# Kernel optimization log

Hardware: AMD Instinct MI355X
Metric: run time of the kernel (lower is better)

## Reference

```python
import jax, jax.numpy as jnp
import numpy as np

GRID_SIZE = 5
SPLINE_ORDER = 3
COEFF = GRID_SIZE + SPLINE_ORDER  # 8 spline coefficients per (out,in) pair
NUM_HEADS = 4
NUM_LAYERS = 4
DIM = 256
FF_DIM = 1024
VOCAB = 32000
EPS_EMB = 1e-12   # layernorm_eps from init
EPS_LN = 1e-5     # nn.LayerNorm default inside encoder layers


def make_grid(in_features):
    # uniform extended B-spline grid over [-1, 1], shape (in, grid_size + 2*order + 1)
    h = 2.0 / GRID_SIZE
    g = jnp.arange(-SPLINE_ORDER, GRID_SIZE + SPLINE_ORDER + 1, dtype=jnp.float32) * h - 1.0
    return jnp.broadcast_to(g, (in_features, g.shape[0]))


def b_splines(x, grid):
    # Cox-de Boor recursion. x: (..., in) -> (..., in, COEFF)
    xe = x[..., None]
    bases = ((xe >= grid[:, :-1]) & (xe < grid[:, 1:])).astype(x.dtype)
    for k in range(1, SPLINE_ORDER + 1):
        left = (xe - grid[:, : -(k + 1)]) / (grid[:, k:-1] - grid[:, : -(k + 1)])
        right = (grid[:, k + 1:] - xe) / (grid[:, k + 1:] - grid[:, 1:-k])
        bases = left * bases[..., :-1] + right * bases[..., 1:]
    return bases


def kan(x, base_w, spline_w):
    # efficient-kan KANLinear: silu base path + B-spline path
    grid = make_grid(x.shape[-1])
    base = jax.nn.silu(x) @ base_w.T
    spl = b_splines(x, grid)                      # (..., in, COEFF)
    return base + jnp.einsum('...ic,oic->...o', spl, spline_w)


def layer_norm(x, g=None, b=None, eps=EPS_LN):
    mu = jnp.mean(x, axis=-1, keepdims=True)
    var = jnp.mean((x - mu) ** 2, axis=-1, keepdims=True)
    y = (x - mu) * jax.lax.rsqrt(var + eps)
    return y * g + b if g is not None else y


def setup_inputs() -> dict:
    key = jax.random.key(0)
    ks = iter(jax.random.split(key, 64))

    def w(shape, s=0.02):
        return jax.random.normal(next(ks), shape, jnp.float32) * s

    inp = {
        'input_ids': jax.random.randint(next(ks), (2, 512), 0, VOCAB),
        'word_emb': w((VOCAB, DIM)),
        'tok_type_emb': w((2, DIM)),
        'pos_emb': w((512, DIM)),
        'emb_ln_g': jnp.ones((DIM,), jnp.float32),
        'emb_ln_b': jnp.zeros((DIM,), jnp.float32),
    }
    L = NUM_LAYERS
    for nm, (o, i) in [('q', (DIM, DIM)), ('k', (DIM, DIM)), ('v', (DIM, DIM)),
                       ('o', (DIM, DIM)), ('f1', (FF_DIM, DIM)), ('f2', (DIM, FF_DIM))]:
        inp[nm + '_base'] = w((L, o, i))
        inp[nm + '_spline'] = w((L, o, i, COEFF))
    inp['ln1_g'] = jnp.ones((L, DIM), jnp.float32)
    inp['ln1_b'] = jnp.zeros((L, DIM), jnp.float32)
    inp['ln2_g'] = jnp.ones((L, DIM), jnp.float32)
    inp['ln2_b'] = jnp.zeros((L, DIM), jnp.float32)
    inp['hk_base'] = w((DIM, DIM))
    inp['hk_spline'] = w((DIM, DIM, COEFF))
    inp['ho_base'] = w((VOCAB, DIM))
    inp['ho_spline'] = w((VOCAB, DIM, COEFF))
    return inp


def reference(input_ids, word_emb, tok_type_emb, pos_emb, emb_ln_g, emb_ln_b,
              q_base, q_spline, k_base, k_spline, v_base, v_spline,
              o_base, o_spline, f1_base, f1_spline, f2_base, f2_spline,
              ln1_g, ln1_b, ln2_g, ln2_b,
              hk_base, hk_spline, ho_base, ho_spline):
    B, S = input_ids.shape
    # Faithful to source: attention_mask defaults to ones_like(input_ids) and is
    # used to index BOTH token-type and positional embedding tables (row 1).
    x = word_emb[input_ids] + tok_type_emb[1] + pos_emb[1]
    x = layer_norm(x, emb_ln_g, emb_ln_b, eps=EPS_EMB)  # dropout = identity (deterministic)

    H, hd = NUM_HEADS, DIM // NUM_HEADS
    scale = hd ** -0.5
    for l in range(NUM_LAYERS):
        def split(t):
            return t.reshape(B, S, H, hd).transpose(0, 2, 1, 3)  # (B,H,S,hd)
        q = split(kan(x, q_base[l], q_spline[l]))
        k = split(kan(x, k_base[l], k_spline[l]))
        v = split(kan(x, v_base[l], v_spline[l]))
        attn = jax.nn.softmax(jnp.einsum('bhqd,bhkd->bhqk', q, k) * scale, axis=-1)
        ctx = jnp.einsum('bhqk,bhkd->bhqd', attn, v).transpose(0, 2, 1, 3).reshape(B, S, DIM)
        x = layer_norm(kan(ctx, o_base[l], o_spline[l]) + x, ln1_g[l], ln1_b[l])
        ff = kan(jax.nn.relu(kan(x, f1_base[l], f1_spline[l])), f2_base[l], f2_spline[l])
        x = layer_norm(ff + x, ln2_g[l], ln2_b[l])

    # GeneratorHead: KAN -> gelu -> layernorm(no affine) -> KAN to vocab
    h = jax.nn.gelu(kan(x, hk_base, hk_spline), approximate=False)
    h = layer_norm(h, eps=EPS_EMB)
    return kan(h, ho_base, ho_spline)  # (B, S, VOCAB)
```

## Files before the change

kernel.cpp:

```cpp
#include <hip/hip_runtime.h>
#include <math.h>

typedef unsigned short u16;
typedef unsigned int u32;
typedef __bf16 bf16x8 __attribute__((ext_vector_type(8)));
typedef float f32x4 __attribute__((ext_vector_type(4)));
typedef u16 us8 __attribute__((ext_vector_type(8)));
typedef u16 us4 __attribute__((ext_vector_type(4)));

#define TOKENS 1024
#define DIM 256
#define SEQ 512


__device__ __forceinline__ u16 f2bf(float f) {
  u32 x = __float_as_uint(f);
  x += 0x7fffu + ((x >> 16) & 1u);
  return (u16)(x >> 16);
}

__device__ __forceinline__ void expand9(float x, u16* sil, us8* u) {
  float sig = 1.0f / (1.0f + expf(-x));
  *sil = f2bf(x * sig);
  float bs[11];
#pragma unroll
  for (int j = 0; j < 11; j++) {
    float gj  = (float)(j - 3) * 0.4f - 1.0f;
    float gj1 = (float)(j - 2) * 0.4f - 1.0f;
    bs[j] = (x >= gj && x < gj1) ? 1.0f : 0.0f;
  }
#pragma unroll
  for (int k = 1; k <= 3; k++) {
#pragma unroll
    for (int j = 0; j < 10; j++) {
      if (j + k < 11) {
        float gj   = (float)(j - 3) * 0.4f - 1.0f;
        float gj1  = (float)(j - 2) * 0.4f - 1.0f;
        float gjk  = (float)(j + k - 3) * 0.4f - 1.0f;
        float gjk1 = (float)(j + k - 2) * 0.4f - 1.0f;
        float linv = 1.0f / (gjk - gj);
        float rinv = 1.0f / (gjk1 - gj1);
        bs[j] = (x - gj) * linv * bs[j] + (gjk1 - x) * rinv * bs[j + 1];
      }
    }
  }
#pragma unroll
  for (int c = 0; c < 8; c++) (*u)[c] = f2bf(bs[c]);
}

__device__ __forceinline__ float block_sum_256(float v) {
  __shared__ float red[4];
  int t = threadIdx.x, lane = t & 63, wid = t >> 6;
#pragma unroll
  for (int o = 32; o > 0; o >>= 1) v += __shfl_down(v, o, 64);
  __syncthreads();
  if (lane == 0) red[wid] = v;
  __syncthreads();
  return red[0] + red[1] + red[2] + red[3];
}

__device__ __forceinline__ float wave_sum_64(float v) {
#pragma unroll
  for (int o = 32; o > 0; o >>= 1) v += __shfl_xor(v, o, 64);
  return v;
}


__global__ void embed_ln_x(const int* __restrict__ ids, const float* __restrict__ wemb,
                           const float* __restrict__ tt, const float* __restrict__ pe,
                           const float* __restrict__ g, const float* __restrict__ bta,
                           float* __restrict__ xout, u16* __restrict__ Xe) {
  int row = blockIdx.x, t = threadIdx.x;
  int id = ids[row];
  float v = wemb[(size_t)id * DIM + t] + tt[DIM + t] + pe[DIM + t];
  float mu = block_sum_256(v) * (1.0f / 256.0f);
  float d = v - mu;
  float var = block_sum_256(d * d) * (1.0f / 256.0f);
  float y = d * rsqrtf(var + 1e-12f) * g[t] + bta[t];
  xout[(size_t)row * DIM + t] = y;
  size_t base = (size_t)row * 2304;
  u16 s; us8 u;
  expand9(y, &s, &u);
  Xe[base + t] = s;
  *(us8*)(Xe + base + 256 + (size_t)t * 8) = u;
}


__global__ void add_ln_x(const float* __restrict__ a, int nsum, int sstride,
                         const float* __restrict__ res,
                         const float* __restrict__ g, const float* __restrict__ bta,
                         float eps, int dogelu,
                         float* __restrict__ xout, u16* __restrict__ Xe) {
  int t = threadIdx.x;
  int row = blockIdx.x * 4 + (t >> 6);
  int lane = t & 63;
  int col = lane * 4;
  int idx = row * 256 + col;
  float4 v = *(const float4*)(a + idx);
  for (int s = 1; s < nsum; s++) {
    float4 p = *(const float4*)(a + (size_t)s * sstride + idx);
    v.x += p.x; v.y += p.y; v.z += p.z; v.w += p.w;
  }
  if (dogelu) {
    const float kk = 0.70710678118654752f;
    v.x = 0.5f * v.x * (1.0f + erff(v.x * kk));
    v.y = 0.5f * v.y * (1.0f + erff(v.y * kk));
    v.z = 0.5f * v.z * (1.0f + erff(v.z * kk));
    v.w = 0.5f * v.w * (1.0f + erff(v.w * kk));
  }
  if (res) {
    float4 rr = *(const float4*)(res + idx);
    v.x += rr.x; v.y += rr.y; v.z += rr.z; v.w += rr.w;
  }
  float mu = wave_sum_64(v.x + v.y + v.z + v.w) * (1.0f / 256.0f);
  float4 d;
  d.x = v.x - mu; d.y = v.y - mu; d.z = v.z - mu; d.w = v.w - mu;
  float var = wave_sum_64(d.x * d.x + d.y * d.y + d.z * d.z + d.w * d.w) * (1.0f / 256.0f);
  float rs = rsqrtf(var + eps);
  float4 y;
  y.x = d.x * rs; y.y = d.y * rs; y.z = d.z * rs; y.w = d.w * rs;
  if (g) {
    float4 gv = *(const float4*)(g + col);
    float4 bv = *(const float4*)(bta + col);
    y.x = y.x * gv.x + bv.x; y.y = y.y * gv.y + bv.y;
    y.z = y.z * gv.z + bv.z; y.w = y.w * gv.w + bv.w;
  }
  *(float4*)(xout + idx) = y;
  size_t base = (size_t)row * 2304;
  u16 s0_, s1_, s2_, s3_;
  us8 u0, u1, u2, u3;
  expand9(y.x, &s0_, &u0);
  expand9(y.y, &s1_, &u1);
  expand9(y.z, &s2_, &u2);
  expand9(y.w, &s3_, &u3);
  us4 sil4; sil4[0] = s0_; sil4[1] = s1_; sil4[2] = s2_; sil4[3] = s3_;
  *(us4*)(Xe + base + col) = sil4;
  *(us8*)(Xe + base + 256 + (size_t)col * 8) = u0;
  *(us8*)(Xe + base + 256 + (size_t)(col + 1) * 8) = u1;
  *(us8*)(Xe + base + 256 + (size_t)(col + 2) * 8) = u2;
  *(us8*)(Xe + base + 256 + (size_t)(col + 3) * 8) = u3;
}


__global__ void expand_ff(const float* __restrict__ X, u16* __restrict__ Xe) {
  int i4 = (blockIdx.x * 256 + threadIdx.x) * 4;
  int n = i4 >> 10, i = i4 & 1023;
  const size_t str = (size_t)TOKENS * 1024;
  float4 v = *(const float4*)(X + i4);
  float4 p1 = *(const float4*)(X + str + i4);
  float4 p2 = *(const float4*)(X + 2 * str + i4);
  v.x = fmaxf(v.x + p1.x + p2.x, 0.0f);
  v.y = fmaxf(v.y + p1.y + p2.y, 0.0f);
  v.z = fmaxf(v.z + p1.z + p2.z, 0.0f);
  v.w = fmaxf(v.w + p1.w + p2.w, 0.0f);
  size_t base = (size_t)n * 9216;
  u16 s0_, s1_, s2_, s3_;
  us8 u0, u1, u2, u3;
  expand9(v.x, &s0_, &u0);
  expand9(v.y, &s1_, &u1);
  expand9(v.z, &s2_, &u2);
  expand9(v.w, &s3_, &u3);
  us4 sil4; sil4[0] = s0_; sil4[1] = s1_; sil4[2] = s2_; sil4[3] = s3_;
  *(us4*)(Xe + base + i) = sil4;
  *(us8*)(Xe + base + 1024 + (size_t)i * 8) = u0;
  *(us8*)(Xe + base + 1024 + (size_t)(i + 1) * 8) = u1;
  *(us8*)(Xe + base + 1024 + (size_t)(i + 2) * 8) = u2;
  *(us8*)(Xe + base + 1024 + (size_t)(i + 3) * 8) = u3;
}


#define LDA4(c, v) { int r_ = (c) * RPC + (t >> LGP); int g_ = t & (GPB - 1); \
    v = *(const uint4*)(A + (size_t)(m0 + r_) * K + k0n + g_ * 8); }
#define LDB4(c, va, vb) { int r_ = (c) * RPC + (t >> LGP); int g_ = t & (GPB - 1); \
    int kv_ = k0n + g_ * 8; \
    const float* p_ = (kv_ < infeat) ? (Wb + (size_t)(onb + r_) * infeat + kv_) \
                                     : (Ws + (size_t)(onb + r_) * infeat * 8 + (kv_ - infeat)); \
    va = *(const float4*)p_; vb = *(const float4*)(p_ + 4); }
#define STA4(c, v) { int r_ = (c) * RPC + (t >> LGP); int g_ = t & (GPB - 1); \
    *(uint4*)(&As[r_ * BK + ((g_ ^ (r_ & (GPB - 1))) << 3)]) = v; }
#define STB4(c, va, vb) { int r_ = (c) * RPC + (t >> LGP); int g_ = t & (GPB - 1); \
    bf16x8 h_; \
    h_[0] = (__bf16)va.x; h_[1] = (__bf16)va.y; h_[2] = (__bf16)va.z; h_[3] = (__bf16)va.w; \
    h_[4] = (__bf16)vb.x; h_[5] = (__bf16)vb.y; h_[6] = (__bf16)vb.z; h_[7] = (__bf16)vb.w; \
    *(bf16x8*)(&Bs[r_ * BK + ((g_ ^ (r_ & (GPB - 1))) << 3)]) = h_; }

template <int BM, int BN, int BK, int MINW, int EPI>
__global__ __launch_bounds__(256, MINW)
void gemm_kw(const u16* __restrict__ A,
             const float* __restrict__ b0, const float* __restrict__ s0,
             const float* __restrict__ b1, const float* __restrict__ s1,
             const float* __restrict__ b2, const float* __restrict__ s2,
             int nper, int N, int K, int infeat, int kchunk, float* __restrict__ C,
             u16* __restrict__ XeOut, int infOut) {
  constexpr int GPB = BK / 8;
  constexpr int LGP = (GPB == 8) ? 3 : 4;
  constexpr int RPC = 256 / GPB;
  static_assert(BM / RPC == 4 && BN / RPC == 4, "need exactly 4+4 chunks");
  constexpr int FM = BM / 32, FN = BN / 32;
  __shared__ u16 As[BM * BK];
  __shared__ u16 Bs[BN * BK];
  const int gx = gridDim.x;
  const int nwg = gx * gridDim.y;
  int g = blockIdx.y * gx + blockIdx.x;
  int lin = g;
  if ((nwg & 7) == 0) lin = (g & 7) * (nwg >> 3) + (g >> 3);
  const int m0 = (lin % gx) * BM;
  const int n0 = (lin / gx) * BN;
  const int z = blockIdx.z;
  const int kbeg = z * kchunk;
  const int kend = (kbeg + kchunk < K) ? kbeg + kchunk : K;
  const int t = threadIdx.x;
  const int lane = t & 63, wid = t >> 6;
  const int wm = (wid >> 1) * (BM / 2), wn = (wid & 1) * (BN / 2);
  const int proj = n0 / nper;
  const float* Wb = proj == 0 ? b0 : (proj == 1 ? b1 : b2);
  const float* Ws = proj == 0 ? s0 : (proj == 1 ? s1 : s2);
  const int onb = n0 - proj * nper;

  f32x4 acc[FM][FN];
#pragma unroll
  for (int i = 0; i < FM; i++)
#pragma unroll
    for (int j = 0; j < FN; j++) acc[i][j] = (f32x4){0.f, 0.f, 0.f, 0.f};

  const int frow = lane & 15;
  const int cgrp = lane >> 4;

  uint4 pa0, pa1, pa2, pa3;
  float4 pb0a, pb0b, pb1a, pb1b, pb2a, pb2b, pb3a, pb3b;
  int k0n = kbeg;
  LDA4(0, pa0); LDA4(1, pa1); LDA4(2, pa2); LDA4(3, pa3);
  LDB4(0, pb0a, pb0b); LDB4(1, pb1a, pb1b); LDB4(2, pb2a, pb2b); LDB4(3, pb3a, pb3b);

  for (int k0 = kbeg; k0 < kend; k0 += BK) {
    STA4(0, pa0); STA4(1, pa1); STA4(2, pa2); STA4(3, pa3);
    STB4(0, pb0a, pb0b); STB4(1, pb1a, pb1b); STB4(2, pb2a, pb2b); STB4(3, pb3a, pb3b);
    __syncthreads();
    if (k0 + BK < kend) {
      k0n = k0 + BK;
      LDA4(0, pa0); LDA4(1, pa1); LDA4(2, pa2); LDA4(3, pa3);
      LDB4(0, pb0a, pb0b); LDB4(1, pb1a, pb1b); LDB4(2, pb2a, pb2b); LDB4(3, pb3a, pb3b);
    }
#pragma unroll
    for (int kk = 0; kk < BK; kk += 32) {
      bf16x8 af[FM], bfr[FN];
#pragma unroll
      for (int i = 0; i < FM; i++) {
        int rr = wm + i * 16 + frow;
        int ch = (kk >> 3) + cgrp;
        af[i] = *reinterpret_cast<const bf16x8*>(&As[rr * BK + ((ch ^ (rr & (GPB - 1))) << 3)]);
      }
#pragma unroll
      for (int j = 0; j < FN; j++) {
        int rr = wn + j * 16 + frow;
        int ch = (kk >> 3) + cgrp;
        bfr[j] = *reinterpret_cast<const bf16x8*>(&Bs[rr * BK + ((ch ^ (rr & (GPB - 1))) << 3)]);
      }
#pragma unroll
      for (int i = 0; i < FM; i++)
#pragma unroll
        for (int j = 0; j < FN; j++)
          acc[i][j] = __builtin_amdgcn_mfma_f32_16x16x32_bf16(af[i], bfr[j], acc[i][j], 0, 0, 0);
    }
    __syncthreads();
  }

  const int crow = (lane >> 4) * 4;
  const int ccol = lane & 15;
  if constexpr (EPI == 0) {
    float* Cz = C + (size_t)z * TOKENS * N;
#pragma unroll
    for (int i = 0; i < FM; i++)
#pragma unroll
      for (int j = 0; j < FN; j++) {
        int row = m0 + wm + i * 16 + crow;
        int col = n0 + wn + j * 16 + ccol;
#pragma unroll
        for (int r = 0; r < 4; r++)
          Cz[(size_t)(row + r) * N + col] = acc[i][j][r];
      }
  } else {
    const int ldXe = infOut * 9;
#pragma unroll
    for (int i = 0; i < FM; i++)
#pragma unroll
      for (int j = 0; j < FN; j++) {
        int row0 = m0 + wm + i * 16 + crow;
        int col = n0 + wn + j * 16 + ccol;
#pragma unroll
        for (int r = 0; r < 4; r++) {
          float y = fmaxf(acc[i][j][r], 0.0f);
          u16 s; us8 u;
          expand9(y, &s, &u);
          size_t base = (size_t)(row0 + r) * ldXe;
          XeOut[base + col] = s;
          *(us8*)(XeOut + base + infOut + (size_t)col * 8) = u;
        }
      }
  }
}


__global__ void attn_fused(const float* __restrict__ qkv, u16* __restrict__ Xe) {
  const float* q1 = qkv + (size_t)TOKENS * 768;
  const float* q2 = qkv + (size_t)2 * TOKENS * 768;
  int bh = blockIdx.x, b = bh >> 2, h = bh & 3;
  int s0 = blockIdx.y * 16;
  int t = threadIdx.x;
  __shared__ float Qs[16][68];
  __shared__ float Ks[32][68];
  __shared__ float Ss[16][513];
  __shared__ float red[16][17];
  __shared__ float Vs[32][68];
  const int srow = t >> 4, sd0 = (t & 15) * 4;
  {
    int rr = t >> 4, d0 = (t & 15) * 4;
    size_t ix = (size_t)(b * SEQ + s0 + rr) * 768 + h * 64 + d0;
    float4 v0 = *(const float4*)(qkv + ix);
    float4 v1 = *(const float4*)(q1 + ix);
    float4 v2 = *(const float4*)(q2 + ix);
    float4 o;
    o.x = v0.x + v1.x + v2.x; o.y = v0.y + v1.y + v2.y;
    o.z = v0.z + v1.z + v2.z; o.w = v0.w + v1.w + v2.w;
    *(float4*)&Qs[rr][d0] = o;
  }
  int r = t >> 4, cc = t & 15;

#define LD32(dst0, dst1, kc, off) { \
    size_t ixa_ = (size_t)(b * SEQ + (kc) + srow) * 768 + (off) + h * 64 + sd0; \
    size_t ixb_ = ixa_ + (size_t)16 * 768; \
    float4 a0_ = *(const float4*)(qkv + ixa_); \
    float4 a1_ = *(const float4*)(q1 + ixa_); \
    float4 a2_ = *(const float4*)(q2 + ixa_); \
    dst0.x = a0_.x + a1_.x + a2_.x; dst0.y = a0_.y + a1_.y + a2_.y; \
    dst0.z = a0_.z + a1_.z + a2_.z; dst0.w = a0_.w + a1_.w + a2_.w; \
    float4 b0_ = *(const float4*)(qkv + ixb_); \
    float4 b1_ = *(const float4*)(q1 + ixb_); \
    float4 b2_ = *(const float4*)(q2 + ixb_); \
    dst1.x = b0_.x + b1_.x + b2_.x; dst1.y = b0_.y + b1_.y + b2_.y; \
    dst1.z = b0_.z + b1_.z + b2_.z; dst1.w = b0_.w + b1_.w + b2_.w; }

  float4 rk0, rk1;
  LD32(rk0, rk1, 0, 256);
  for (int tile = 0; tile < 16; tile++) {
    *(float4*)&Ks[srow][sd0] = rk0;
    *(float4*)&Ks[16 + srow][sd0] = rk1;
    __syncthreads();
    if (tile < 15) LD32(rk0, rk1, (tile + 1) * 32, 256);
    int colbase = tile * 32;
#pragma unroll
    for (int c2 = 0; c2 < 2; c2++) {
      int col = cc + c2 * 16;
      float acc = 0.f;
#pragma unroll
      for (int d4 = 0; d4 < 16; d4++) {
        float4 qv = *(const float4*)&Qs[r][d4 * 4];
        float4 kv = *(const float4*)&Ks[col][d4 * 4];
        acc += qv.x * kv.x;
        acc += qv.y * kv.y;
        acc += qv.z * kv.z;
        acc += qv.w * kv.w;
      }
      Ss[r][colbase + col] = acc * 0.125f;
    }
    __syncthreads();
  }
  float mx = -3.4e38f;
  for (int j = cc; j < SEQ; j += 16) mx = fmaxf(mx, Ss[r][j]);
  red[r][cc] = mx;
  __syncthreads();
  if (cc == 0) {
    float m = red[r][0];
#pragma unroll
    for (int j = 1; j < 16; j++) m = fmaxf(m, red[r][j]);
    red[r][16] = m;
  }
  __syncthreads();
  mx = red[r][16];
  float sm = 0.f;
  for (int j = cc; j < SEQ; j += 16) {
    float e = expf(Ss[r][j] - mx);
    Ss[r][j] = e;
    sm += e;
  }
  __syncthreads();
  red[r][cc] = sm;
  __syncthreads();
  if (cc == 0) {
    float s = 0.f;
#pragma unroll
    for (int j = 0; j < 16; j++) s += red[r][j];
    red[r][16] = s;
  }
  __syncthreads();
  float inv = 1.0f / red[r][16];
  for (int j = cc; j < SEQ; j += 16) Ss[r][j] *= inv;
  int dd = cc * 4;
  float a0 = 0.f, a1 = 0.f, a2 = 0.f, a3 = 0.f;
  float4 rv0, rv1;
  LD32(rv0, rv1, 0, 512);
  for (int tile = 0; tile < 16; tile++) {
    *(float4*)&Vs[srow][sd0] = rv0;
    *(float4*)&Vs[16 + srow][sd0] = rv1;
    __syncthreads();
    if (tile < 15) LD32(rv0, rv1, (tile + 1) * 32, 512);
    int kc = tile * 32;
#pragma unroll
    for (int kk = 0; kk < 32; kk++) {
      float p = Ss[r][kc + kk];
      float4 vv = *(const float4*)&Vs[kk][dd];
      a0 += p * vv.x;
      a1 += p * vv.y;
      a2 += p * vv.z;
      a3 += p * vv.w;
    }
    __syncthreads();
  }
#undef LD32
  int row = b * SEQ + s0 + r;
  size_t base = (size_t)row * 2304;
  float av[4] = {a0, a1, a2, a3};
#pragma unroll
  for (int j = 0; j < 4; j++) {
    int col = h * 64 + dd + j;
    u16 s; us8 u;
    expand9(av[j], &s, &u);
    Xe[base + col] = s;
    *(us8*)(Xe + base + 256 + (size_t)col * 8) = u;
  }
}


extern "C" void kernel_launch(void* const* d_in, const int* in_sizes, int n_in,
                              void* d_out, int out_size, void* d_ws, size_t ws_size,
                              hipStream_t stream) {
  const int* ids = (const int*)d_in[0];
  const float* wemb = (const float*)d_in[1];
  const float* ttemb = (const float*)d_in[2];
  const float* pemb = (const float*)d_in[3];
  const float* elg = (const float*)d_in[4];
  const float* elb = (const float*)d_in[5];
  const float* qb = (const float*)d_in[6], *qs = (const float*)d_in[7];
  const float* kb = (const float*)d_in[8], *ks = (const float*)d_in[9];
  const float* vb = (const float*)d_in[10], *vs = (const float*)d_in[11];
  const float* ob = (const float*)d_in[12], *osp = (const float*)d_in[13];
  const float* f1b = (const float*)d_in[14], *f1s = (const float*)d_in[15];
  const float* f2b = (const float*)d_in[16], *f2s = (const float*)d_in[17];
  const float* l1g = (const float*)d_in[18], *l1b = (const float*)d_in[19];
  const float* l2g = (const float*)d_in[20], *l2b = (const float*)d_in[21];
  const float* hkb = (const float*)d_in[22], *hks = (const float*)d_in[23];
  const float* hob = (const float*)d_in[24], *hos = (const float*)d_in[25];
  float* out = (float*)d_out;

  char* w = (char*)d_ws;
  const size_t MB = 1 << 20;
  float* xbuf = (float*)(w);
  float* tmp  = (float*)(w + 1 * MB);
  float* qkv  = (float*)(w + 2 * MB);
  float* part = (float*)(w + 11 * MB);
  u16*   Xe2  = (u16*)  (w + 20 * MB);
  u16*   Xe   = (u16*)  (w + 38 * MB);
  float* f1p  = (float*)(w + 43 * MB);

  embed_ln_x<<<TOKENS, 256, 0, stream>>>(ids, wemb, ttemb, pemb, elg, elb, xbuf, Xe);

  for (int l = 0; l < 4; l++) {
    const float* qbl = qb + (size_t)l * 65536, *qsl = qs + (size_t)l * 524288;
    const float* kbl = kb + (size_t)l * 65536, *ksl = ks + (size_t)l * 524288;
    const float* vbl = vb + (size_t)l * 65536, *vsl = vs + (size_t)l * 524288;
    const float* obl = ob + (size_t)l * 65536, *osl = osp + (size_t)l * 524288;
    const float* f1bl = f1b + (size_t)l * 262144, *f1sl = f1s + (size_t)l * 2097152;
    const float* f2bl = f2b + (size_t)l * 262144, *f2sl = f2s + (size_t)l * 2097152;

    gemm_kw<64, 64, 128, 2, 0><<<dim3(16, 12, 3), 256, 0, stream>>>(
        Xe, qbl, qsl, kbl, ksl, vbl, vsl, 256, 768, 2304, 256, 768, qkv, nullptr, 0);
    attn_fused<<<dim3(8, 32), 256, 0, stream>>>(qkv, Xe);
    gemm_kw<64, 64, 128, 2, 0><<<dim3(16, 4, 9), 256, 0, stream>>>(
        Xe, obl, osl, obl, osl, obl, osl, 256, 256, 2304, 256, 256, part, nullptr, 0);
    add_ln_x<<<TOKENS / 4, 256, 0, stream>>>(part, 9, TOKENS * 256, xbuf,
                                             l1g + l * 256, l1b + l * 256, 1e-5f, 0, xbuf, Xe);
    gemm_kw<64, 64, 128, 2, 0><<<dim3(16, 16, 3), 256, 0, stream>>>(
        Xe, f1bl, f1sl, f1bl, f1sl, f1bl, f1sl, 1024, 1024, 2304, 256, 768,
        f1p, nullptr, 0);
    expand_ff<<<1024, 256, 0, stream>>>(f1p, Xe2);
    gemm_kw<64, 64, 128, 2, 0><<<dim3(16, 4, 8), 256, 0, stream>>>(
        Xe2, f2bl, f2sl, f2bl, f2sl, f2bl, f2sl, 256, 256, 9216, 1024, 1152,
        part, nullptr, 0);
    add_ln_x<<<TOKENS / 4, 256, 0, stream>>>(part, 8, TOKENS * 256, xbuf,
                                             l2g + l * 256, l2b + l * 256, 1e-5f, 0, xbuf, Xe);
  }

  gemm_kw<64, 64, 128, 2, 0><<<dim3(16, 4, 9), 256, 0, stream>>>(
      Xe, hkb, hks, hkb, hks, hkb, hks, 256, 256, 2304, 256, 256, part, nullptr, 0);
  add_ln_x<<<TOKENS / 4, 256, 0, stream>>>(part, 9, TOKENS * 256, nullptr, nullptr, nullptr,
                                           1e-12f, 1, tmp, Xe);
  gemm_kw<128, 128, 64, 1, 0><<<dim3(8, 250), 256, 0, stream>>>(
      Xe, hob, hos, hob, hos, hob, hos, 32000, 32000, 2304, 256, 2304, out, nullptr, 0);
}
```

Measured before the change: 780.5 us.

## Add dedicated vocab-head GEMM using direct global-to-LDS loads with swizzled tiles

Replaces the generic templated GEMM for the final 256->32000 KAN output projection with a specialized kernel. Tiles of A (bf16) and fp32 weights are loaded straight into LDS via global_load_lds in 16-byte chunks, with XOR swizzling to avoid bank conflicts. Blocks are remapped in groups of eight for better L2 locality. B is kept in fp32 in LDS and converted to bf16 at fragment load, which doubles LDS footprint, and there is no double buffering.

```diff
diff --git a/kernel.cpp b/kernel.cpp
--- a/kernel.cpp
+++ b/kernel.cpp
@@ -17,6 +17,12 @@
   u32 x = __float_as_uint(f);
   x += 0x7fffu + ((x >> 16) & 1u);
   return (u16)(x >> 16);
+}
+
+__device__ __forceinline__ void gload16(const void* g, void* l) {
+  __builtin_amdgcn_global_load_lds(
+      (const __attribute__((address_space(1))) void*)g,
+      (__attribute__((address_space(3))) void*)l, 16, 0, 0);
 }
 
 __device__ __forceinline__ void expand9(float x, u16* sil, us8* u) {
@@ -301,6 +307,102 @@
 }
 
 
+__global__ __launch_bounds__(256, 1)
+void gemm_hob(const u16* __restrict__ A,
+              const float* __restrict__ Wb, const float* __restrict__ Ws,
+              int N, int K, int infeat, float* __restrict__ C) {
+  __shared__ u16 As[128 * 64];
+  __shared__ float Bsf[128 * 64];
+  const int gx = gridDim.x;
+  const int nwg = gx * gridDim.y;
+  int g = blockIdx.y * gx + blockIdx.x;
+  int lin = (g & 7) * (nwg >> 3) + (g >> 3);
+  const int m0 = (lin % gx) * 128;
+  const int n0 = (lin / gx) * 128;
+  const int t = threadIdx.x;
+  const int lane = t & 63, wid = t >> 6;
+  const int wm = (wid >> 1) * 64, wn = (wid & 1) * 64;
+  const int frow = lane & 15;
+  const int cgrp = lane >> 4;
+
+  f32x4 acc[4][4];
+#pragma unroll
+  for (int i = 0; i < 4; i++)
+#pragma unroll
+    for (int j = 0; j < 4; j++) acc[i][j] = (f32x4){0.f, 0.f, 0.f, 0.f};
+
+  const int rAw = lane >> 3;
+  const int gA = (lane & 7) ^ rAw;
+  const int rBw = lane >> 4;
+  const int jB = lane & 15;
+
+  for (int k0 = 0; k0 < K; k0 += 64) {
+#pragma unroll
+    for (int c = 0; c < 4; c++) {
+      int rA = c * 32 + wid * 8 + rAw;
+      const u16* src = A + (size_t)(m0 + rA) * K + k0 + gA * 8;
+      u16* dst = As + ((size_t)(c * 32 + wid * 8) << 6) + lane * 8;
+      gload16(src, dst);
+    }
+#pragma unroll
+    for (int c = 0; c < 4; c++)
+#pragma unroll
+      for (int q = 0; q < 2; q++) {
+        int rB = c * 32 + wid * 8 + q * 4 + rBw;
+        int jsrc = jB ^ (((wid * 8 + q * 4) & 15) + rBw);
+        int kv = k0 + jsrc * 4;
+        const float* src = (kv < infeat)
+            ? (Wb + (size_t)(n0 + rB) * infeat + kv)
+            : (Ws + (size_t)(n0 + rB) * (size_t)infeat * 8 + (kv - infeat));
+        float* dst = Bsf + ((size_t)(c * 32 + wid * 8 + q * 4) << 6) + lane * 4;
+        gload16(src, dst);
+      }
+    __syncthreads();
+#pragma unroll
+    for (int half = 0; half < 2; half++) {
+      const int ch = half * 4 + cgrp;
+      bf16x8 af[4], bfr[4];
+#pragma unroll
+      for (int i = 0; i < 4; i++) {
+        int rr = wm + i * 16 + frow;
+        af[i] = *reinterpret_cast<const bf16x8*>(&As[(rr << 6) + ((ch ^ (rr & 7)) << 3)]);
+      }
+#pragma unroll
+      for (int j = 0; j < 4; j++) {
+        int rr = wn + j * 16 + frow;
+        int sl0 = (2 * ch) ^ (rr & 15);
+        int sl1 = (2 * ch + 1) ^ (rr & 15);
+        float4 f0 = *reinterpret_cast<const float4*>(&Bsf[(rr << 6) + sl0 * 4]);
+        float4 f1 = *reinterpret_cast<const float4*>(&Bsf[(rr << 6) + sl1 * 4]);
+        bf16x8 h;
+        h[0] = (__bf16)f0.x; h[1] = (__bf16)f0.y; h[2] = (__bf16)f0.z; h[3] = (__bf16)f0.w;
+        h[4] = (__bf16)f1.x; h[5] = (__bf16)f1.y; h[6] = (__bf16)f1.z; h[7] = (__bf16)f1.w;
+        bfr[j] = h;
+      }
+#pragma unroll
+      for (int i = 0; i < 4; i++)
+#pragma unroll
+        for (int j = 0; j < 4; j++)
+          acc[i][j] = __builtin_amdgcn_mfma_f32_16x16x32_bf16(af[i], bfr[j], acc[i][j], 0, 0, 0);
+    }
+    __syncthreads();
+  }
+
+  const int crow = (lane >> 4) * 4;
+  const int ccol = lane & 15;
+#pragma unroll
+  for (int i = 0; i < 4; i++)
+#pragma unroll
+    for (int j = 0; j < 4; j++) {
+      int row = m0 + wm + i * 16 + crow;
+      int col = n0 + wn + j * 16 + ccol;
+#pragma unroll
+      for (int r = 0; r < 4; r++)
+        C[(size_t)(row + r) * N + col] = acc[i][j][r];
+    }
+}
+
+
 __global__ void attn_fused(const float* __restrict__ qkv, u16* __restrict__ Xe) {
   const float* q1 = qkv + (size_t)TOKENS * 768;
   const float* q2 = qkv + (size_t)2 * TOKENS * 768;
@@ -494,6 +596,5 @@
       Xe, hkb, hks, hkb, hks, hkb, hks, 256, 256, 2304, 256, 256, part, nullptr, 0);
   add_ln_x<<<TOKENS / 4, 256, 0, stream>>>(part, 9, TOKENS * 256, nullptr, nullptr, nullptr,
                                            1e-12f, 1, tmp, Xe);
-  gemm_kw<128, 128, 64, 1, 0><<<dim3(8, 250), 256, 0, stream>>>(
-      Xe, hob, hos, hob, hos, hob, hos, 32000, 32000, 2304, 256, 2304, out, nullptr, 0);
-}
+  gemm_hob<<<dim3(8, 250), 256, 0, stream>>>(Xe, hob, hos, 32000, 2304, 256, out);
+}
```

Result: slower. 874.9 us (+12.1%).

## Double-buffer shared memory tiles in KAN GEMM to drop one barrier per k-step

Applied to the files above, without the earlier changes.

The GEMM main loop now keeps two shared-memory buffers for the A and B tiles. It stores the next tile into the alternate buffer while computing on the current one, which removes one __syncthreads per k iteration and lets the LDS writes overlap the MFMA work. Shared memory use doubles, which may lower occupancy for the larger tile configurations. Global loads for tile k+2 are still held in registers.

```diff
diff --git a/kernel.cpp b/kernel.cpp
--- a/kernel.cpp
+++ b/kernel.cpp
@@ -176,13 +176,18 @@
     const float* p_ = (kv_ < infeat) ? (Wb + (size_t)(onb + r_) * infeat + kv_) \
                                      : (Ws + (size_t)(onb + r_) * infeat * 8 + (kv_ - infeat)); \
     va = *(const float4*)p_; vb = *(const float4*)(p_ + 4); }
-#define STA4(c, v) { int r_ = (c) * RPC + (t >> LGP); int g_ = t & (GPB - 1); \
-    *(uint4*)(&As[r_ * BK + ((g_ ^ (r_ & (GPB - 1))) << 3)]) = v; }
-#define STB4(c, va, vb) { int r_ = (c) * RPC + (t >> LGP); int g_ = t & (GPB - 1); \
+#define STA4(dst, c, v) { int r_ = (c) * RPC + (t >> LGP); int g_ = t & (GPB - 1); \
+    *(uint4*)(&(dst)[r_ * BK + ((g_ ^ (r_ & (GPB - 1))) << 3)]) = v; }
+#define STB4(dst, c, va, vb) { int r_ = (c) * RPC + (t >> LGP); int g_ = t & (GPB - 1); \
     bf16x8 h_; \
     h_[0] = (__bf16)va.x; h_[1] = (__bf16)va.y; h_[2] = (__bf16)va.z; h_[3] = (__bf16)va.w; \
     h_[4] = (__bf16)vb.x; h_[5] = (__bf16)vb.y; h_[6] = (__bf16)vb.z; h_[7] = (__bf16)vb.w; \
-    *(bf16x8*)(&Bs[r_ * BK + ((g_ ^ (r_ & (GPB - 1))) << 3)]) = h_; }
+    *(bf16x8*)(&(dst)[r_ * BK + ((g_ ^ (r_ & (GPB - 1))) << 3)]) = h_; }
+
+#define LOAD_ALL { LDA4(0, pa0); LDA4(1, pa1); LDA4(2, pa2); LDA4(3, pa3); \
+    LDB4(0, pb0a, pb0b); LDB4(1, pb1a, pb1b); LDB4(2, pb2a, pb2b); LDB4(3, pb3a, pb3b); }
+#define STORE_ALL(ad, bd) { STA4(ad, 0, pa0); STA4(ad, 1, pa1); STA4(ad, 2, pa2); STA4(ad, 3, pa3); \
+    STB4(bd, 0, pb0a, pb0b); STB4(bd, 1, pb1a, pb1b); STB4(bd, 2, pb2a, pb2b); STB4(bd, 3, pb3a, pb3b); }
 
 template <int BM, int BN, int BK, int MINW, int EPI>
 __global__ __launch_bounds__(256, MINW)
@@ -197,8 +202,8 @@
   constexpr int RPC = 256 / GPB;
   static_assert(BM / RPC == 4 && BN / RPC == 4, "need exactly 4+4 chunks");
   constexpr int FM = BM / 32, FN = BN / 32;
-  __shared__ u16 As[BM * BK];
-  __shared__ u16 Bs[BN * BK];
+  __shared__ u16 As[2][BM * BK];
+  __shared__ u16 Bs[2][BN * BK];
   const int gx = gridDim.x;
   const int nwg = gx * gridDim.y;
   int g = blockIdx.y * gx + blockIdx.x;
@@ -228,19 +233,23 @@
 
   uint4 pa0, pa1, pa2, pa3;
   float4 pb0a, pb0b, pb1a, pb1b, pb2a, pb2b, pb3a, pb3b;
+  const int nk = (kend - kbeg) / BK;
   int k0n = kbeg;
-  LDA4(0, pa0); LDA4(1, pa1); LDA4(2, pa2); LDA4(3, pa3);
-  LDB4(0, pb0a, pb0b); LDB4(1, pb1a, pb1b); LDB4(2, pb2a, pb2b); LDB4(3, pb3a, pb3b);
-
-  for (int k0 = kbeg; k0 < kend; k0 += BK) {
-    STA4(0, pa0); STA4(1, pa1); STA4(2, pa2); STA4(3, pa3);
-    STB4(0, pb0a, pb0b); STB4(1, pb1a, pb1b); STB4(2, pb2a, pb2b); STB4(3, pb3a, pb3b);
-    __syncthreads();
-    if (k0 + BK < kend) {
-      k0n = k0 + BK;
-      LDA4(0, pa0); LDA4(1, pa1); LDA4(2, pa2); LDA4(3, pa3);
-      LDB4(0, pb0a, pb0b); LDB4(1, pb1a, pb1b); LDB4(2, pb2a, pb2b); LDB4(3, pb3a, pb3b);
+  LOAD_ALL;
+  STORE_ALL(As[0], Bs[0]);
+  if (nk > 1) { k0n = kbeg + BK; LOAD_ALL; }
+  __syncthreads();
+
+  int p = 0;
+  for (int ki = 0; ki < nk; ki++) {
+    if (ki + 1 < nk) {
+      u16* an = &As[p ^ 1][0];
+      u16* bn = &Bs[p ^ 1][0];
+      STORE_ALL(an, bn);
+      if (ki + 2 < nk) { k0n = kbeg + (ki + 2) * BK; LOAD_ALL; }
     }
+    const u16* ac = &As[p][0];
+    const u16* bc = &Bs[p][0];
 #pragma unroll
     for (int kk = 0; kk < BK; kk += 32) {
       bf16x8 af[FM], bfr[FN];
@@ -248,13 +257,13 @@
       for (int i = 0; i < FM; i++) {
         int rr = wm + i * 16 + frow;
         int ch = (kk >> 3) + cgrp;
-        af[i] = *reinterpret_cast<const bf16x8*>(&As[rr * BK + ((ch ^ (rr & (GPB - 1))) << 3)]);
+        af[i] = *reinterpret_cast<const bf16x8*>(&ac[rr * BK + ((ch ^ (rr & (GPB - 1))) << 3)]);
       }
 #pragma unroll
       for (int j = 0; j < FN; j++) {
         int rr = wn + j * 16 + frow;
         int ch = (kk >> 3) + cgrp;
-        bfr[j] = *reinterpret_cast<const bf16x8*>(&Bs[rr * BK + ((ch ^ (rr & (GPB - 1))) << 3)]);
+        bfr[j] = *reinterpret_cast<const bf16x8*>(&bc[rr * BK + ((ch ^ (rr & (GPB - 1))) << 3)]);
       }
 #pragma unroll
       for (int i = 0; i < FM; i++)
@@ -263,6 +272,7 @@
           acc[i][j] = __builtin_amdgcn_mfma_f32_16x16x32_bf16(af[i], bfr[j], acc[i][j], 0, 0, 0);
     }
     __syncthreads();
+    p ^= 1;
   }
 
   const int crow = (lane >> 4) * 4;
```

New measurement: 802.0 us. 1.03x slower.
